# Kernel tuning notes

Hardware: AMD Instinct MI355X
Metric: run time of the kernel (lower is better)

Reference implementation:

```python
import math
import jax, jax.numpy as jnp
import numpy as np

D_MODEL, N_HEADS, D_HEAD, D_INNER = 512, 8, 64, 2048
QLEN, MLEN, BATCH = 2048, 2048, 2


def _layernorm(x, g, b, eps=1e-5):
    mu = jnp.mean(x, axis=-1, keepdims=True)
    var = jnp.var(x, axis=-1, keepdims=True)
    return (x - mu) * jax.lax.rsqrt(var + eps) * g + b


def _rel_shift(x):
    # x: [qlen, klen, B, n] -> Transformer-XL relative shift
    q, k, b, n = x.shape
    x = jnp.pad(x, ((0, 0), (1, 0), (0, 0), (0, 0)))  # zero-pad key dim at front
    x = x.reshape(k + 1, q, b, n)[1:].reshape(q, k, b, n)
    return x


def setup_inputs() -> dict:
    key = jax.random.key(0)
    ks = jax.random.split(key, 16)
    nd = N_HEADS * D_HEAD
    s = 0.02
    return {
        "x": jax.random.normal(ks[0], (QLEN, BATCH, D_MODEL), jnp.float32),
        "r": jax.random.normal(ks[1], (QLEN + MLEN, D_MODEL), jnp.float32),
        "u": jax.random.normal(ks[2], (N_HEADS, D_HEAD), jnp.float32) * s,
        "v": jax.random.normal(ks[3], (N_HEADS, D_HEAD), jnp.float32) * s,
        "mems": jax.random.normal(ks[4], (MLEN, BATCH, D_MODEL), jnp.float32),
        "Wqkv": jax.random.normal(ks[5], (3 * nd, D_MODEL), jnp.float32) * s,
        "Wr": jax.random.normal(ks[6], (nd, D_MODEL), jnp.float32) * s,
        "Wo": jax.random.normal(ks[7], (D_MODEL, nd), jnp.float32) * s,
        "ln1_g": jnp.ones((D_MODEL,), jnp.float32),
        "ln1_b": jnp.zeros((D_MODEL,), jnp.float32),
        "W1": jax.random.normal(ks[8], (D_MODEL, D_INNER), jnp.float32) * s,
        "b1": jnp.zeros((D_INNER,), jnp.float32),
        "W2": jax.random.normal(ks[9], (D_INNER, D_MODEL), jnp.float32) * s,
        "b2": jnp.zeros((D_MODEL,), jnp.float32),
        "ln2_g": jnp.ones((D_MODEL,), jnp.float32),
        "ln2_b": jnp.zeros((D_MODEL,), jnp.float32),
    }


def reference(x, r, u, v, mems, Wqkv, Wr, Wo, ln1_g, ln1_b, W1, b1, W2, b2, ln2_g, ln2_b):
    qlen, B, d_model = x.shape
    n_heads, d_head = u.shape
    cat = jnp.concatenate([mems, x], axis=0)          # [klen, B, d_model]
    klen = cat.shape[0]
    mlen = klen - qlen

    qkv = cat @ Wqkv.T                                 # [klen, B, 3*n*d]
    q, k, val = jnp.split(qkv, 3, axis=-1)
    q = q[-qlen:].reshape(qlen, B, n_heads, d_head)
    k = k.reshape(klen, B, n_heads, d_head)
    val = val.reshape(klen, B, n_heads, d_head)
    rk = (r @ Wr.T).reshape(klen, n_heads, d_head)     # relative key heads

    AC = jnp.einsum('ibnd,jbnd->ijbn', q + u, k)       # content score
    BD = _rel_shift(jnp.einsum('ibnd,jnd->ijbn', q + v, rk))  # position score
    score = (AC + BD) * (1.0 / math.sqrt(d_head))      # [qlen, klen, B, n]

    # causal mask with memory: query i attends keys j <= i + mlen
    mask = jnp.arange(klen)[None, :] > (jnp.arange(qlen)[:, None] + mlen)
    score = jnp.where(mask[:, :, None, None], jnp.float32(-1e30), score)
    attn = jax.nn.softmax(score, axis=1)

    out = jnp.einsum('ijbn,jbnd->ibnd', attn, val).reshape(qlen, B, n_heads * d_head)
    out = out @ Wo.T
    h = _layernorm(x + out, ln1_g, ln1_b)              # post-LN attention

    core = jax.nn.relu(h @ W1 + b1) @ W2 + b2          # PositionwiseFF
    return _layernorm(h + core, ln2_g, ln2_b)
```

## Files before the change

### kernel.cpp

```cpp
#include <hip/hip_runtime.h>
#include <hip/hip_bf16.h>

#define QLEN 2048
#define MLEN 2048
#define KLEN 4096
#define BATCH 2
#define DMODEL 512
#define NHEADS 8
#define DHEAD 64
#define DINNER 2048

typedef __attribute__((ext_vector_type(8))) short  vs8;
typedef __attribute__((ext_vector_type(8))) __bf16 vbf8;
typedef __attribute__((ext_vector_type(4))) float  vf4;

__device__ __forceinline__ float bf2f(ushort h) {
    union { unsigned u; float f; } c; c.u = ((unsigned)h) << 16; return c.f;
}
__device__ __forceinline__ ushort f2bf(float f) {
    union { float f; unsigned u; } c; c.f = f;
    unsigned u = c.u;
    return (ushort)((u + 0x7FFFu + ((u >> 16) & 1u)) >> 16);
}
__device__ __forceinline__ vf4 mfma16(vs8 a, vs8 b, vf4 c) {
    return __builtin_amdgcn_mfma_f32_16x16x32_bf16(
        __builtin_bit_cast(vbf8, a), __builtin_bit_cast(vbf8, b), c, 0, 0, 0);
}
__device__ __forceinline__ void gl16(const ushort* g, ushort* l) {
    __builtin_amdgcn_global_load_lds(
        (const __attribute__((address_space(1))) void*)g,
        (__attribute__((address_space(3))) void*)l, 16, 0, 0);
}

__global__ void cvt_bf(const float* __restrict__ in, ushort* __restrict__ out, int nel4) {
    int i = blockIdx.x * 256 + threadIdx.x;
    if (i < nel4) {
        float4 f = ((const float4*)in)[i];
        ushort4 o; o.x = f2bf(f.x); o.y = f2bf(f.y); o.z = f2bf(f.z); o.w = f2bf(f.w);
        ((ushort4*)out)[i] = o;
    }
}

__global__ void cvt_cat(const float* __restrict__ mems, const float* __restrict__ x,
                        ushort* __restrict__ out) {
    int i = blockIdx.x * 256 + threadIdx.x;
    const int half4 = MLEN * BATCH * DMODEL / 4;
    if (i < 2 * half4) {
        float4 f = (i < half4) ? ((const float4*)mems)[i] : ((const float4*)x)[i - half4];
        ushort4 o; o.x = f2bf(f.x); o.y = f2bf(f.y); o.z = f2bf(f.z); o.w = f2bf(f.w);
        ((ushort4*)out)[i] = o;
    }
}

__global__ void cvt_tr(const float* __restrict__ in, ushort* __restrict__ out, int R, int C) {
    __shared__ float t[32][33];
    const int c0 = blockIdx.x * 32, r0 = blockIdx.y * 32;
    const int tx = threadIdx.x & 31, ty = threadIdx.x >> 5;
#pragma unroll
    for (int q = 0; q < 4; ++q) {
        int r = ty + q * 8;
        t[r][tx] = in[(size_t)(r0 + r) * C + c0 + tx];
    }
    __syncthreads();
#pragma unroll
    for (int q = 0; q < 4; ++q) {
        int c = ty + q * 8;
        out[(size_t)(c0 + c) * R + r0 + tx] = f2bf(t[tx][c]);
    }
}

__global__ void vtrans(const ushort* __restrict__ qkv, ushort* __restrict__ vT) {
    __shared__ __align__(16) ushort t_lds[64][72];
    const int j0 = blockIdx.x * 64, n = blockIdx.y, b = blockIdx.z;
    const int tid = threadIdx.x;
#pragma unroll
    for (int p = 0; p < 2; ++p) {
        int u2 = p * 256 + tid;
        int j = u2 >> 3, d8 = (u2 & 7) * 8;
        vs8 v8 = *(const vs8*)(qkv + ((size_t)(j0 + j) * BATCH + b) * 1536 + 1024 + n * 64 + d8);
#pragma unroll
        for (int e = 0; e < 8; ++e) t_lds[d8 + e][j] = (ushort)v8[e];
    }
    __syncthreads();
#pragma unroll
    for (int p = 0; p < 2; ++p) {
        int u2 = p * 256 + tid;
        int d = u2 >> 3, j8 = (u2 & 7) * 8;
        vs8 o8 = *(const vs8*)&t_lds[d][j8];
        *(vs8*)(vT + ((size_t)(b * NHEADS + n) * 64 + d) * KLEN + j0 + j8) = o8;
    }
}

template <int EPI>
__global__ __launch_bounds__(256)
void gemm_bt(const ushort* __restrict__ A, const ushort* __restrict__ B,
             void* __restrict__ C0, void* __restrict__ C1,
             const float* __restrict__ bias, int M, int N, int K, int kc) {
    __shared__ __align__(16) ushort As[128 * 32];
    __shared__ __align__(16) ushort Bs[128 * 32];
    const int n0 = blockIdx.x * 128;
    const int m0 = blockIdx.y * 128;
    const int kb = blockIdx.z * kc;
    void* C = blockIdx.z ? C1 : C0;
    const int tid = threadIdx.x;
    const int lane = tid & 63, wave = tid >> 6;
    const int wr = wave >> 1, wc = wave & 1;
    const int lr = lane & 15, lg = lane >> 4;
    vf4 acc[4][4] = {};

    for (int k0 = kb; k0 < kb + kc; k0 += 32) {
        __syncthreads();
#pragma unroll
        for (int t = 0; t < 2; ++t) {
            int u = t * 256 + tid;
            int row = u >> 2, cu = u & 3;
            int sc = cu ^ ((row >> 1) & 3);
            ushort* la = As + t * 2048 + (tid & 192) * 8;
            ushort* lb = Bs + t * 2048 + (tid & 192) * 8;
            gl16(&A[(size_t)(m0 + row) * K + k0 + sc * 8], la);
            gl16(&B[(size_t)(n0 + row) * K + k0 + sc * 8], lb);
        }
        __syncthreads();
        vs8 af[4], bfr[4];
#pragma unroll
        for (int m = 0; m < 4; ++m) {
            int rr = wr * 64 + m * 16 + lr;
            af[m] = *(const vs8*)&As[rr * 32 + (lg ^ ((rr >> 1) & 3)) * 8];
        }
#pragma unroll
        for (int nn = 0; nn < 4; ++nn) {
            int rr = wc * 64 + nn * 16 + lr;
            bfr[nn] = *(const vs8*)&Bs[rr * 32 + (lg ^ ((rr >> 1) & 3)) * 8];
        }
#pragma unroll
        for (int m = 0; m < 4; ++m)
#pragma unroll
            for (int nn = 0; nn < 4; ++nn)
                acc[m][nn] = mfma16(af[m], bfr[nn], acc[m][nn]);
    }

#pragma unroll
    for (int m = 0; m < 4; ++m) {
#pragma unroll
        for (int nn = 0; nn < 4; ++nn) {
            int row0 = m0 + wr * 64 + m * 16 + lg * 4;
            int col  = n0 + wc * 64 + nn * 16 + lr;
#pragma unroll
            for (int rr = 0; rr < 4; ++rr) {
                float vv = acc[m][nn][rr];
                size_t off = (size_t)(row0 + rr) * N + col;
                if (EPI == 0) ((float*)C)[off] = vv;
                else if (EPI == 1) ((ushort*)C)[off] = f2bf(vv);
                else {
                    float t2 = vv + bias[col];
                    ((ushort*)C)[off] = f2bf(t2 > 0.f ? t2 : 0.f);
                }
            }
        }
    }
}

__global__ __launch_bounds__(256, 4)
void attn2(const ushort* __restrict__ qkv, const ushort* __restrict__ rkp,
           const ushort* __restrict__ vT, const float* __restrict__ uu,
           const float* __restrict__ vv, float* __restrict__ part_l,
           float* __restrict__ part_o) {
    __shared__ __align__(16) ushort K_lds[64 * 64];
    __shared__ __align__(16) ushort V_lds[64 * 64];
    __shared__ __align__(16) ushort w_lds[4][16 * 84];
    __shared__ __align__(16) ushort p_lds[4][16 * 72];

    const int chunk = blockIdx.x & 1, qb = blockIdx.x >> 1;
    const int b = blockIdx.y, n = blockIdx.z;
    const int tid = threadIdx.x, lane = tid & 63, w = tid >> 6;
    const int lr = lane & 15, lg = lane >> 4;
    const int i0w = qb * 64 + w * 16;

    ushort* wl = w_lds[w];
    ushort* pl = p_lds[w];

    vs8 aqu[2], aqv[2];
#pragma unroll
    for (int kk = 0; kk < 2; ++kk) {
        int d0 = kk * 32 + lg * 8;
        vs8 q8 = *(const vs8*)(qkv + ((size_t)(i0w + lr + MLEN) * BATCH + b) * 1536 + n * 64 + d0);
#pragma unroll
        for (int e = 0; e < 8; ++e) {
            float qf = bf2f((ushort)q8[e]);
            aqu[kk][e] = (short)f2bf(qf + uu[n * 64 + d0 + e]);
            aqv[kk][e] = (short)f2bf(qf + vv[n * 64 + d0 + e]);
        }
    }

    const vf4 zero4 = {0.f, 0.f, 0.f, 0.f};
    vf4 o[4] = {zero4, zero4, zero4, zero4};
    float l_run[4] = {0.f, 0.f, 0.f, 0.f};

    const int jstart = chunk ? 2048 : 0;
    const int niter = chunk ? (qb + 1) : 32;
    const ushort* vTh = vT + (size_t)(b * NHEADS + n) * 64 * KLEN;

    for (int it = 0; it < niter; ++it) {
        const int j0 = jstart + it * 64;
        __syncthreads();
#pragma unroll
        for (int p = 0; p < 2; ++p) {
            int u2 = p * 256 + tid;
            int row = u2 >> 3, cb = u2 & 7;
            int sc = (cb + row) & 7;
            *(vs8*)&K_lds[row * 64 + sc * 8] =
                *(const vs8*)(qkv + ((size_t)(j0 + row) * BATCH + b) * 1536 + 512 + n * 64 + cb * 8);
            *(vs8*)&V_lds[row * 64 + sc * 8] =
                *(const vs8*)(vTh + (size_t)row * KLEN + j0 + cb * 8);
        }
        __syncthreads();

        vf4 acc_s[4] = {zero4, zero4, zero4, zero4};
#pragma unroll
        for (int q = 0; q < 4; ++q) {
            int jr = q * 16 + lr;
#pragma unroll
            for (int kk = 0; kk < 2; ++kk) {
                vs8 kb = *(const vs8*)&K_lds[jr * 64 + ((kk * 4 + lg + jr) & 7) * 8];
                acc_s[q] = mfma16(aqu[kk], kb, acc_s[q]);
            }
        }
        const int mbase = j0 - i0w + 2032;
#pragma unroll
        for (int wg = 0; wg < 5; ++wg) {
            vf4 aw = zero4;
            int mrow = mbase + wg * 16 + lr;
            mrow = mrow > KLEN - 1 ? KLEN - 1 : mrow;
#pragma unroll
            for (int kk = 0; kk < 2; ++kk) {
                vs8 rb = *(const vs8*)(rkp + (size_t)mrow * 512 + n * 64 + kk * 32 + lg * 8);
                aw = mfma16(aqv[kk], rb, aw);
            }
#pragma unroll
            for (int r = 0; r < 4; ++r)
                wl[(lg * 4 + r) * 84 + wg * 16 + lr] = f2bf(aw[r]);
        }
        const int jmi = j0 - i0w - 2048;
#pragma unroll
        for (int r = 0; r < 4; ++r) {
            int il = lg * 4 + r;
            float p4[4], psum = 0.f;
#pragma unroll
            for (int q = 0; q < 4; ++q) {
                int jl = q * 16 + lr;
                float s = (acc_s[q][r] + bf2f(wl[il * 84 + jl - il + 15])) * 0.125f;
                if (jl - il + jmi > 0) s = -1e30f;
                p4[q] = __expf(s);
                psum += p4[q];
            }
#pragma unroll
            for (int off = 1; off < 16; off <<= 1) psum += __shfl_xor(psum, off);
            l_run[r] += psum;
#pragma unroll
            for (int q = 0; q < 4; ++q) pl[il * 72 + q * 16 + lr] = f2bf(p4[q]);
        }
#pragma unroll
        for (int jk = 0; jk < 2; ++jk) {
            vs8 pf = *(const vs8*)&pl[lr * 72 + jk * 32 + lg * 8];
#pragma unroll
            for (int dg = 0; dg < 4; ++dg) {
                int dr = dg * 16 + lr;
                vs8 vfr = *(const vs8*)&V_lds[dr * 64 + ((jk * 4 + lg + dr) & 7) * 8];
                o[dg] = mfma16(pf, vfr, o[dg]);
            }
        }
    }

#pragma unroll
    for (int r = 0; r < 4; ++r) {
        int i = i0w + lg * 4 + r;
        int pr = (i * 2 + b) * 8 + n;
        size_t base = ((size_t)chunk * 32768 + pr) * 64;
#pragma unroll
        for (int dg = 0; dg < 4; ++dg)
            part_o[base + dg * 16 + lr] = o[dg][r];
        if (lr == 0) part_l[chunk * 32768 + pr] = l_run[r];
    }
}

__global__ __launch_bounds__(256)
void combine(const float* __restrict__ part_l, const float* __restrict__ part_o,
             ushort* __restrict__ ao) {
    int t = blockIdx.x * 256 + threadIdx.x;
    int pr = t >> 6, d = t & 63;
    float l = part_l[pr] + part_l[32768 + pr];
    float ov = part_o[(size_t)pr * 64 + d] + part_o[(size_t)(32768 + pr) * 64 + d];
    int i2b = pr >> 3, n = pr & 7;
    ao[(size_t)i2b * 512 + n * 64 + d] = f2bf(ov / l);
}

__global__ __launch_bounds__(64)
void ln_fuse(const float* __restrict__ base, const float* __restrict__ pa,
             const float* __restrict__ pb, const float* __restrict__ bias,
             const float* __restrict__ g, const float* __restrict__ bb,
             float* __restrict__ of32, ushort* __restrict__ obf) {
    const int row = blockIdx.x;
    const int lane = threadIdx.x;
    const size_t off0 = (size_t)row * DMODEL + lane * 8;
    float vals[8];
    float s = 0.f, s2 = 0.f;
#pragma unroll
    for (int e = 0; e < 8; ++e) {
        float t = base[off0 + e] + pa[off0 + e];
        if (pb) t += pb[off0 + e];
        if (bias) t += bias[lane * 8 + e];
        vals[e] = t; s += t; s2 += t * t;
    }
#pragma unroll
    for (int o = 1; o < 64; o <<= 1) { s += __shfl_xor(s, o); s2 += __shfl_xor(s2, o); }
    const float mean = s * (1.f / DMODEL);
    const float var = s2 * (1.f / DMODEL) - mean * mean;
    const float rstd = rsqrtf(var + 1e-5f);
#pragma unroll
    for (int e = 0; e < 8; ++e) {
        int c = lane * 8 + e;
        float y = (vals[e] - mean) * rstd * g[c] + bb[c];
        if (of32) of32[(size_t)row * DMODEL + c] = y;
        if (obf)  obf[(size_t)row * DMODEL + c] = f2bf(y);
    }
}

extern "C" void kernel_launch(void* const* d_in, const int* in_sizes, int n_in,
                              void* d_out, int out_size, void* d_ws, size_t ws_size,
                              hipStream_t stream) {
    const float* x    = (const float*)d_in[0];
    const float* r    = (const float*)d_in[1];
    const float* u    = (const float*)d_in[2];
    const float* v    = (const float*)d_in[3];
    const float* mems = (const float*)d_in[4];
    const float* Wqkv = (const float*)d_in[5];
    const float* Wr   = (const float*)d_in[6];
    const float* Wo   = (const float*)d_in[7];
    const float* ln1g = (const float*)d_in[8];
    const float* ln1b = (const float*)d_in[9];
    const float* W1   = (const float*)d_in[10];
    const float* b1   = (const float*)d_in[11];
    const float* W2   = (const float*)d_in[12];
    const float* b2   = (const float*)d_in[13];
    const float* ln2g = (const float*)d_in[14];
    const float* ln2b = (const float*)d_in[15];
    float* out = (float*)d_out;

    char* p = (char*)d_ws;
    auto alloc = [&](size_t bytes) { char* q = p; p += (bytes + 255) & ~(size_t)255; return q; };
    ushort* cat_bf  = (ushort*)alloc((size_t)KLEN * BATCH * DMODEL * 2);
    ushort* wqkv_bf = (ushort*)alloc((size_t)1536 * 512 * 2);
    ushort* r_bf    = (ushort*)alloc((size_t)KLEN * 512 * 2);
    ushort* wr_bf   = (ushort*)alloc((size_t)512 * 512 * 2);
    ushort* wo_bf   = (ushort*)alloc((size_t)512 * 512 * 2);
    ushort* w1t_bf  = (ushort*)alloc((size_t)DINNER * 512 * 2);
    ushort* w2t_bf  = (ushort*)alloc((size_t)512 * DINNER * 2);
    ushort* qkv_bf  = (ushort*)alloc((size_t)KLEN * BATCH * 1536 * 2);
    ushort* rk_bf   = (ushort*)alloc((size_t)KLEN * 512 * 2);
    ushort* vT      = (ushort*)alloc((size_t)BATCH * NHEADS * 64 * KLEN * 2);
    ushort* ao_bf   = (ushort*)alloc((size_t)QLEN * BATCH * 512 * 2);
    ushort* h_bf    = (ushort*)alloc((size_t)QLEN * BATCH * 512 * 2);
    ushort* ff1_bf  = (ushort*)alloc((size_t)QLEN * BATCH * DINNER * 2);
    float*  proj1a  = (float*)alloc((size_t)QLEN * BATCH * 512 * 4);
    float*  proj1b  = (float*)alloc((size_t)QLEN * BATCH * 512 * 4);
    float*  h_f32   = (float*)alloc((size_t)QLEN * BATCH * 512 * 4);
    float* part_l = (float*)cat_bf;
    float* part_o = (float*)ff1_bf;
    float* proj2a = proj1a;
    float* proj2b = proj1b;

    const int MROWS = QLEN * BATCH;
    const int CATROWS = KLEN * BATCH;

    cvt_cat<<<(CATROWS * DMODEL / 4 + 255) / 256, 256, 0, stream>>>(mems, x, cat_bf);
    cvt_bf<<<(KLEN * 512 / 4 + 255) / 256, 256, 0, stream>>>(r, r_bf, KLEN * 512 / 4);
    cvt_bf<<<(1536 * 512 / 4 + 255) / 256, 256, 0, stream>>>(Wqkv, wqkv_bf, 1536 * 512 / 4);
    cvt_bf<<<(512 * 512 / 4 + 255) / 256, 256, 0, stream>>>(Wr, wr_bf, 512 * 512 / 4);
    cvt_bf<<<(512 * 512 / 4 + 255) / 256, 256, 0, stream>>>(Wo, wo_bf, 512 * 512 / 4);
    cvt_tr<<<dim3(DINNER / 32, 512 / 32), 256, 0, stream>>>(W1, w1t_bf, 512, DINNER);
    cvt_tr<<<dim3(512 / 32, DINNER / 32), 256, 0, stream>>>(W2, w2t_bf, DINNER, 512);

    gemm_bt<1><<<dim3(1536 / 128, CATROWS / 128, 1), 256, 0, stream>>>(
        cat_bf, wqkv_bf, qkv_bf, nullptr, nullptr, CATROWS, 1536, 512, 512);
    gemm_bt<1><<<dim3(512 / 128, KLEN / 128, 1), 256, 0, stream>>>(
        r_bf, wr_bf, rk_bf, nullptr, nullptr, KLEN, 512, 512, 512);

    vtrans<<<dim3(KLEN / 64, NHEADS, BATCH), 256, 0, stream>>>(qkv_bf, vT);
    attn2<<<dim3(64, BATCH, NHEADS), 256, 0, stream>>>(qkv_bf, rk_bf, vT, u, v, part_l, part_o);
    combine<<<32768 * 64 / 256, 256, 0, stream>>>(part_l, part_o, ao_bf);

    gemm_bt<0><<<dim3(512 / 128, MROWS / 128, 2), 256, 0, stream>>>(
        ao_bf, wo_bf, proj1a, proj1b, nullptr, MROWS, 512, 512, 256);
    ln_fuse<<<MROWS, 64, 0, stream>>>(x, proj1a, proj1b, nullptr, ln1g, ln1b, h_f32, h_bf);

    gemm_bt<2><<<dim3(DINNER / 128, MROWS / 128, 1), 256, 0, stream>>>(
        h_bf, w1t_bf, ff1_bf, nullptr, b1, MROWS, DINNER, 512, 512);
    gemm_bt<0><<<dim3(512 / 128, MROWS / 128, 2), 256, 0, stream>>>(
        ff1_bf, w2t_bf, proj2a, proj2b, nullptr, MROWS, 512, 2048, 1024);
    ln_fuse<<<MROWS, 64, 0, stream>>>(h_f32, proj2a, proj2b, b2, ln2g, ln2b, out, nullptr);
}
```

Measured before the change: 345.9 us.

## Double-buffer GEMM and attention tiles, head-major rk layout, and cheaper epilogues

The GEMM and attention kernels now double-buffer their LDS tiles, loading with global_load_lds and waiting on vmcnt so the next tile's load overlaps the current MFMAs. The rk projection is written head-major so the position-score loads are contiguous, and the softmax scale is folded into q. Causal masking runs only on the diagonal tile. Several smaller kernels are also changed: combine and ln_fuse are vectorised or packed into larger blocks, and f2bf uses the native bf16 convert. Doubling the LDS buffers and lowering attn occupancy to 3 blocks may cost occupancy, and the hand-counted vmcnt waits are fragile.

```diff
diff --git a/kernel.cpp b/kernel.cpp
--- a/kernel.cpp
+++ b/kernel.cpp
@@ -18,9 +18,7 @@
     union { unsigned u; float f; } c; c.u = ((unsigned)h) << 16; return c.f;
 }
 __device__ __forceinline__ ushort f2bf(float f) {
-    union { float f; unsigned u; } c; c.f = f;
-    unsigned u = c.u;
-    return (ushort)((u + 0x7FFFu + ((u >> 16) & 1u)) >> 16);
+    return __builtin_bit_cast(unsigned short, (__bf16)f);
 }
 __device__ __forceinline__ vf4 mfma16(vs8 a, vs8 b, vf4 c) {
     return __builtin_amdgcn_mfma_f32_16x16x32_bf16(
@@ -30,6 +28,13 @@
     __builtin_amdgcn_global_load_lds(
         (const __attribute__((address_space(1))) void*)g,
         (__attribute__((address_space(3))) void*)l, 16, 0, 0);
+}
+#define WAITV4 asm volatile("s_waitcnt vmcnt(4)" ::: "memory")
+#define WAITV0 asm volatile("s_waitcnt vmcnt(0)" ::: "memory")
+__device__ __forceinline__ void barx() {
+    asm volatile("" ::: "memory");
+    __builtin_amdgcn_s_barrier();
+    asm volatile("" ::: "memory");
 }
 
 __global__ void cvt_bf(const float* __restrict__ in, ushort* __restrict__ out, int nel4) {
@@ -96,8 +101,8 @@
 void gemm_bt(const ushort* __restrict__ A, const ushort* __restrict__ B,
              void* __restrict__ C0, void* __restrict__ C1,
              const float* __restrict__ bias, int M, int N, int K, int kc) {
-    __shared__ __align__(16) ushort As[128 * 32];
-    __shared__ __align__(16) ushort Bs[128 * 32];
+    __shared__ __align__(16) ushort As[2][128 * 32];
+    __shared__ __align__(16) ushort Bs[2][128 * 32];
     const int n0 = blockIdx.x * 128;
     const int m0 = blockIdx.y * 128;
     const int kb = blockIdx.z * kc;
@@ -108,35 +113,44 @@
     const int lr = lane & 15, lg = lane >> 4;
     vf4 acc[4][4] = {};
 
-    for (int k0 = kb; k0 < kb + kc; k0 += 32) {
-        __syncthreads();
+    auto stage = [&](int bi, int k0) {
 #pragma unroll
         for (int t = 0; t < 2; ++t) {
             int u = t * 256 + tid;
             int row = u >> 2, cu = u & 3;
             int sc = cu ^ ((row >> 1) & 3);
-            ushort* la = As + t * 2048 + (tid & 192) * 8;
-            ushort* lb = Bs + t * 2048 + (tid & 192) * 8;
-            gl16(&A[(size_t)(m0 + row) * K + k0 + sc * 8], la);
-            gl16(&B[(size_t)(n0 + row) * K + k0 + sc * 8], lb);
-        }
-        __syncthreads();
+            gl16(&A[(size_t)(m0 + row) * K + k0 + sc * 8],
+                 &As[bi][t * 2048 + (tid & 192) * 8]);
+            gl16(&B[(size_t)(n0 + row) * K + k0 + sc * 8],
+                 &Bs[bi][t * 2048 + (tid & 192) * 8]);
+        }
+    };
+
+    const int nt = kc >> 5;
+    stage(0, kb);
+    int cur = 0;
+    for (int t = 0; t < nt; ++t) {
+        if (t + 1 < nt) { stage(cur ^ 1, kb + (t + 1) * 32); WAITV4; }
+        else { WAITV0; }
+        barx();
         vs8 af[4], bfr[4];
 #pragma unroll
         for (int m = 0; m < 4; ++m) {
             int rr = wr * 64 + m * 16 + lr;
-            af[m] = *(const vs8*)&As[rr * 32 + (lg ^ ((rr >> 1) & 3)) * 8];
+            af[m] = *(const vs8*)&As[cur][rr * 32 + (lg ^ ((rr >> 1) & 3)) * 8];
         }
 #pragma unroll
         for (int nn = 0; nn < 4; ++nn) {
             int rr = wc * 64 + nn * 16 + lr;
-            bfr[nn] = *(const vs8*)&Bs[rr * 32 + (lg ^ ((rr >> 1) & 3)) * 8];
+            bfr[nn] = *(const vs8*)&Bs[cur][rr * 32 + (lg ^ ((rr >> 1) & 3)) * 8];
         }
 #pragma unroll
         for (int m = 0; m < 4; ++m)
 #pragma unroll
             for (int nn = 0; nn < 4; ++nn)
                 acc[m][nn] = mfma16(af[m], bfr[nn], acc[m][nn]);
+        barx();
+        cur ^= 1;
     }
 
 #pragma unroll
@@ -151,22 +165,25 @@
                 size_t off = (size_t)(row0 + rr) * N + col;
                 if (EPI == 0) ((float*)C)[off] = vv;
                 else if (EPI == 1) ((ushort*)C)[off] = f2bf(vv);
-                else {
+                else if (EPI == 2) {
                     float t2 = vv + bias[col];
                     ((ushort*)C)[off] = f2bf(t2 > 0.f ? t2 : 0.f);
+                } else {
+                    ((ushort*)C)[(((size_t)(col >> 6)) << 18) + (size_t)(row0 + rr) * 64 + (col & 63)]
+                        = f2bf(vv);
                 }
             }
         }
     }
 }
 
-__global__ __launch_bounds__(256, 4)
-void attn2(const ushort* __restrict__ qkv, const ushort* __restrict__ rkp,
+__global__ __launch_bounds__(256, 3)
+void attn2(const ushort* __restrict__ qkv, const ushort* __restrict__ rkh,
            const ushort* __restrict__ vT, const float* __restrict__ uu,
            const float* __restrict__ vv, float* __restrict__ part_l,
            float* __restrict__ part_o) {
-    __shared__ __align__(16) ushort K_lds[64 * 64];
-    __shared__ __align__(16) ushort V_lds[64 * 64];
+    __shared__ __align__(16) ushort K_lds[2][64 * 64];
+    __shared__ __align__(16) ushort V_lds[2][64 * 64];
     __shared__ __align__(16) ushort w_lds[4][16 * 84];
     __shared__ __align__(16) ushort p_lds[4][16 * 72];
 
@@ -178,6 +195,8 @@
 
     ushort* wl = w_lds[w];
     ushort* pl = p_lds[w];
+    const ushort* rh  = rkh + ((size_t)n << 18);
+    const ushort* vTh = vT + (size_t)(b * NHEADS + n) * 64 * KLEN;
 
     vs8 aqu[2], aqv[2];
 #pragma unroll
@@ -187,8 +206,8 @@
 #pragma unroll
         for (int e = 0; e < 8; ++e) {
             float qf = bf2f((ushort)q8[e]);
-            aqu[kk][e] = (short)f2bf(qf + uu[n * 64 + d0 + e]);
-            aqv[kk][e] = (short)f2bf(qf + vv[n * 64 + d0 + e]);
+            aqu[kk][e] = (short)f2bf((qf + uu[n * 64 + d0 + e]) * 0.125f);
+            aqv[kk][e] = (short)f2bf((qf + vv[n * 64 + d0 + e]) * 0.125f);
         }
     }
 
@@ -198,22 +217,26 @@
 
     const int jstart = chunk ? 2048 : 0;
     const int niter = chunk ? (qb + 1) : 32;
-    const ushort* vTh = vT + (size_t)(b * NHEADS + n) * 64 * KLEN;
-
+
+    auto stagekv = [&](int bi, int j0) {
+#pragma unroll
+        for (int p = 0; p < 2; ++p) {
+            int row = p * 32 + w * 8 + (lane >> 3);
+            int g = ((lane & 7) - row) & 7;
+            gl16(qkv + ((size_t)(j0 + row) * BATCH + b) * 1536 + 512 + n * 64 + g * 8,
+                 &K_lds[bi][p * 2048 + w * 512]);
+            gl16(vTh + (size_t)row * KLEN + j0 + g * 8,
+                 &V_lds[bi][p * 2048 + w * 512]);
+        }
+    };
+
+    stagekv(0, jstart);
+    int cur = 0;
     for (int it = 0; it < niter; ++it) {
         const int j0 = jstart + it * 64;
-        __syncthreads();
-#pragma unroll
-        for (int p = 0; p < 2; ++p) {
-            int u2 = p * 256 + tid;
-            int row = u2 >> 3, cb = u2 & 7;
-            int sc = (cb + row) & 7;
-            *(vs8*)&K_lds[row * 64 + sc * 8] =
-                *(const vs8*)(qkv + ((size_t)(j0 + row) * BATCH + b) * 1536 + 512 + n * 64 + cb * 8);
-            *(vs8*)&V_lds[row * 64 + sc * 8] =
-                *(const vs8*)(vTh + (size_t)row * KLEN + j0 + cb * 8);
-        }
-        __syncthreads();
+        if (it + 1 < niter) { stagekv(cur ^ 1, j0 + 64); WAITV4; }
+        else { WAITV0; }
+        barx();
 
         vf4 acc_s[4] = {zero4, zero4, zero4, zero4};
 #pragma unroll
@@ -221,7 +244,7 @@
             int jr = q * 16 + lr;
 #pragma unroll
             for (int kk = 0; kk < 2; ++kk) {
-                vs8 kb = *(const vs8*)&K_lds[jr * 64 + ((kk * 4 + lg + jr) & 7) * 8];
+                vs8 kb = *(const vs8*)&K_lds[cur][jr * 64 + ((kk * 4 + lg + jr) & 7) * 8];
                 acc_s[q] = mfma16(aqu[kk], kb, acc_s[q]);
             }
         }
@@ -233,42 +256,63 @@
             mrow = mrow > KLEN - 1 ? KLEN - 1 : mrow;
 #pragma unroll
             for (int kk = 0; kk < 2; ++kk) {
-                vs8 rb = *(const vs8*)(rkp + (size_t)mrow * 512 + n * 64 + kk * 32 + lg * 8);
+                vs8 rb = *(const vs8*)(rh + (size_t)mrow * 64 + kk * 32 + lg * 8);
                 aw = mfma16(aqv[kk], rb, aw);
             }
 #pragma unroll
             for (int r = 0; r < 4; ++r)
                 wl[(lg * 4 + r) * 84 + wg * 16 + lr] = f2bf(aw[r]);
         }
-        const int jmi = j0 - i0w - 2048;
-#pragma unroll
-        for (int r = 0; r < 4; ++r) {
-            int il = lg * 4 + r;
-            float p4[4], psum = 0.f;
-#pragma unroll
-            for (int q = 0; q < 4; ++q) {
-                int jl = q * 16 + lr;
-                float s = (acc_s[q][r] + bf2f(wl[il * 84 + jl - il + 15])) * 0.125f;
-                if (jl - il + jmi > 0) s = -1e30f;
-                p4[q] = __expf(s);
-                psum += p4[q];
-            }
-#pragma unroll
-            for (int off = 1; off < 16; off <<= 1) psum += __shfl_xor(psum, off);
-            l_run[r] += psum;
-#pragma unroll
-            for (int q = 0; q < 4; ++q) pl[il * 72 + q * 16 + lr] = f2bf(p4[q]);
-        }
+
+        const bool domask = chunk && (it == niter - 1);
+        if (!domask) {
+#pragma unroll
+            for (int r = 0; r < 4; ++r) {
+                int il = lg * 4 + r;
+                float psum = 0.f;
+#pragma unroll
+                for (int q = 0; q < 4; ++q) {
+                    int jl = q * 16 + lr;
+                    float p4 = __expf(acc_s[q][r] + bf2f(wl[il * 84 + jl - il + 15]));
+                    psum += p4;
+                    pl[il * 72 + jl] = f2bf(p4);
+                }
+#pragma unroll
+                for (int off = 1; off < 16; off <<= 1) psum += __shfl_xor(psum, off);
+                l_run[r] += psum;
+            }
+        } else {
+#pragma unroll
+            for (int r = 0; r < 4; ++r) {
+                int il = lg * 4 + r;
+                float psum = 0.f;
+#pragma unroll
+                for (int q = 0; q < 4; ++q) {
+                    int jl = q * 16 + lr;
+                    float s = acc_s[q][r] + bf2f(wl[il * 84 + jl - il + 15]);
+                    if (jl - il > w * 16) s = -1e30f;
+                    float p4 = __expf(s);
+                    psum += p4;
+                    pl[il * 72 + jl] = f2bf(p4);
+                }
+#pragma unroll
+                for (int off = 1; off < 16; off <<= 1) psum += __shfl_xor(psum, off);
+                l_run[r] += psum;
+            }
+        }
+
 #pragma unroll
         for (int jk = 0; jk < 2; ++jk) {
             vs8 pf = *(const vs8*)&pl[lr * 72 + jk * 32 + lg * 8];
 #pragma unroll
             for (int dg = 0; dg < 4; ++dg) {
                 int dr = dg * 16 + lr;
-                vs8 vfr = *(const vs8*)&V_lds[dr * 64 + ((jk * 4 + lg + dr) & 7) * 8];
+                vs8 vfr = *(const vs8*)&V_lds[cur][dr * 64 + ((jk * 4 + lg + dr) & 7) * 8];
                 o[dg] = mfma16(pf, vfr, o[dg]);
             }
         }
+        barx();
+        cur ^= 1;
     }
 
 #pragma unroll
@@ -287,20 +331,26 @@
 void combine(const float* __restrict__ part_l, const float* __restrict__ part_o,
              ushort* __restrict__ ao) {
     int t = blockIdx.x * 256 + threadIdx.x;
-    int pr = t >> 6, d = t & 63;
+    int pr = t >> 4, d4 = (t & 15) * 4;
     float l = part_l[pr] + part_l[32768 + pr];
-    float ov = part_o[(size_t)pr * 64 + d] + part_o[(size_t)(32768 + pr) * 64 + d];
+    float4 a = *(const float4*)&part_o[(size_t)pr * 64 + d4];
+    float4 c = *(const float4*)&part_o[(size_t)(32768 + pr) * 64 + d4];
+    float rl = 1.f / l;
     int i2b = pr >> 3, n = pr & 7;
-    ao[(size_t)i2b * 512 + n * 64 + d] = f2bf(ov / l);
-}
-
-__global__ __launch_bounds__(64)
+    ushort* dst = ao + (size_t)i2b * 512 + n * 64 + d4;
+    dst[0] = f2bf((a.x + c.x) * rl);
+    dst[1] = f2bf((a.y + c.y) * rl);
+    dst[2] = f2bf((a.z + c.z) * rl);
+    dst[3] = f2bf((a.w + c.w) * rl);
+}
+
+__global__ __launch_bounds__(256)
 void ln_fuse(const float* __restrict__ base, const float* __restrict__ pa,
              const float* __restrict__ pb, const float* __restrict__ bias,
              const float* __restrict__ g, const float* __restrict__ bb,
              float* __restrict__ of32, ushort* __restrict__ obf) {
-    const int row = blockIdx.x;
-    const int lane = threadIdx.x;
+    const int row = blockIdx.x * 4 + (threadIdx.x >> 6);
+    const int lane = threadIdx.x & 63;
     const size_t off0 = (size_t)row * DMODEL + lane * 8;
     float vals[8];
     float s = 0.f, s2 = 0.f;
@@ -356,7 +406,7 @@
     ushort* w1t_bf  = (ushort*)alloc((size_t)DINNER * 512 * 2);
     ushort* w2t_bf  = (ushort*)alloc((size_t)512 * DINNER * 2);
     ushort* qkv_bf  = (ushort*)alloc((size_t)KLEN * BATCH * 1536 * 2);
-    ushort* rk_bf   = (ushort*)alloc((size_t)KLEN * 512 * 2);
+    ushort* rkh_bf  = (ushort*)alloc((size_t)KLEN * 512 * 2);
     ushort* vT      = (ushort*)alloc((size_t)BATCH * NHEADS * 64 * KLEN * 2);
     ushort* ao_bf   = (ushort*)alloc((size_t)QLEN * BATCH * 512 * 2);
     ushort* h_bf    = (ushort*)alloc((size_t)QLEN * BATCH * 512 * 2);
@@ -382,20 +432,20 @@
 
     gemm_bt<1><<<dim3(1536 / 128, CATROWS / 128, 1), 256, 0, stream>>>(
         cat_bf, wqkv_bf, qkv_bf, nullptr, nullptr, CATROWS, 1536, 512, 512);
-    gemm_bt<1><<<dim3(512 / 128, KLEN / 128, 1), 256, 0, stream>>>(
-        r_bf, wr_bf, rk_bf, nullptr, nullptr, KLEN, 512, 512, 512);
+    gemm_bt<3><<<dim3(512 / 128, KLEN / 128, 1), 256, 0, stream>>>(
+        r_bf, wr_bf, rkh_bf, nullptr, nullptr, KLEN, 512, 512, 512);
 
     vtrans<<<dim3(KLEN / 64, NHEADS, BATCH), 256, 0, stream>>>(qkv_bf, vT);
-    attn2<<<dim3(64, BATCH, NHEADS), 256, 0, stream>>>(qkv_bf, rk_bf, vT, u, v, part_l, part_o);
-    combine<<<32768 * 64 / 256, 256, 0, stream>>>(part_l, part_o, ao_bf);
+    attn2<<<dim3(64, BATCH, NHEADS), 256, 0, stream>>>(qkv_bf, rkh_bf, vT, u, v, part_l, part_o);
+    combine<<<32768 * 16 / 256, 256, 0, stream>>>(part_l, part_o, ao_bf);
 
     gemm_bt<0><<<dim3(512 / 128, MROWS / 128, 2), 256, 0, stream>>>(
         ao_bf, wo_bf, proj1a, proj1b, nullptr, MROWS, 512, 512, 256);
-    ln_fuse<<<MROWS, 64, 0, stream>>>(x, proj1a, proj1b, nullptr, ln1g, ln1b, h_f32, h_bf);
+    ln_fuse<<<MROWS / 4, 256, 0, stream>>>(x, proj1a, proj1b, nullptr, ln1g, ln1b, h_f32, h_bf);
 
     gemm_bt<2><<<dim3(DINNER / 128, MROWS / 128, 1), 256, 0, stream>>>(
         h_bf, w1t_bf, ff1_bf, nullptr, b1, MROWS, DINNER, 512, 512);
     gemm_bt<0><<<dim3(512 / 128, MROWS / 128, 2), 256, 0, stream>>>(
         ff1_bf, w2t_bf, proj2a, proj2b, nullptr, MROWS, 512, 2048, 1024);
-    ln_fuse<<<MROWS, 64, 0, stream>>>(h_f32, proj2a, proj2b, b2, ln2g, ln2b, out, nullptr);
-}
+    ln_fuse<<<MROWS / 4, 256, 0, stream>>>(h_f32, proj2a, proj2b, b2, ln2g, ln2b, out, nullptr);
+}
```

New measurement: 367.4 us. 6.2% more time.
